# Kernel optimization log

Measured on AMD Instinct MI355X. Metric: run time of the kernel, lower is better.

The kernel has to match this reference:

```python
import jax, jax.numpy as jnp
import numpy as np
from jax import lax

NUM_HEADS = 3
HEAD_CH = 64  # in_ch // num_heads = 192 // 3
EPS = 1e-5   # haiku BatchNorm default eps


def _conv_proj(x, dw, scale, offset, pw, stride):
    # DepthwiseConv2D (SAME, no bias) -> BatchNorm (training: batch stats) -> 1x1 Conv (no bias)
    C = x.shape[-1]
    x = lax.conv_general_dilated(
        x, dw, (stride, stride), 'SAME',
        dimension_numbers=('NHWC', 'HWIO', 'NHWC'),
        feature_group_count=C)
    mean = x.mean(axis=(0, 1, 2))
    var = x.var(axis=(0, 1, 2))
    x = (x - mean) * lax.rsqrt(var + EPS) * scale + offset
    return jnp.einsum('bhwc,cd->bhwd', x, pw)  # pointwise 1x1 conv


def _split_heads(x):
    # b H W (h d) -> b h (H W) d
    b, hh, ww, c = x.shape
    return x.reshape(b, hh * ww, NUM_HEADS, HEAD_CH).transpose(0, 2, 1, 3)


def setup_inputs() -> dict:
    key = jax.random.key(0)
    ks = jax.random.split(key, 18)
    B, H, W, C = 16, 56, 56, 192
    Cout = NUM_HEADS * HEAD_CH  # 192
    g = lambda k, shape, s=0.02: jax.random.normal(k, shape, jnp.float32) * s
    return {
        'inputs_q':  jax.random.normal(ks[0], (B, H, W, C), jnp.float32),
        'inputs_kv': jax.random.normal(ks[1], (B, H, W, C), jnp.float32),
        # depthwise kernels (k, k, 1, C)
        'dw_q': g(ks[2], (3, 3, 1, C)), 'dw_k': g(ks[3], (3, 3, 1, C)), 'dw_v': g(ks[4], (3, 3, 1, C)),
        # BN scale/offset per projection
        'scale_q': jnp.ones((C,), jnp.float32), 'offset_q': jnp.zeros((C,), jnp.float32),
        'scale_k': jnp.ones((C,), jnp.float32), 'offset_k': jnp.zeros((C,), jnp.float32),
        'scale_v': jnp.ones((C,), jnp.float32), 'offset_v': jnp.zeros((C,), jnp.float32),
        # pointwise 1x1 conv kernels (C, Cout)
        'pw_q': g(ks[5], (C, Cout)), 'pw_k': g(ks[6], (C, Cout)), 'pw_v': g(ks[7], (C, Cout)),
        # talking-heads mixing matrices (h, h), near-identity init
        'pre_sm':  jnp.eye(NUM_HEADS, dtype=jnp.float32) + g(ks[8], (NUM_HEADS, NUM_HEADS), 0.1),
        'post_sm': jnp.eye(NUM_HEADS, dtype=jnp.float32) + g(ks[9], (NUM_HEADS, NUM_HEADS), 0.1),
        # output linear (no bias)
        'w_out': g(ks[10], (Cout, C)),
    }


def reference(inputs_q, inputs_kv, dw_q, dw_k, dw_v,
              scale_q, offset_q, scale_k, offset_k, scale_v, offset_v,
              pw_q, pw_k, pw_v, pre_sm, post_sm, w_out):
    q = _conv_proj(inputs_q,  dw_q, scale_q, offset_q, pw_q, 1)  # [B,56,56,192]
    k = _conv_proj(inputs_kv, dw_k, scale_k, offset_k, pw_k, 2)  # [B,28,28,192]
    v = _conv_proj(inputs_kv, dw_v, scale_v, offset_v, pw_v, 2)
    B = q.shape[0]
    q = _split_heads(q) / jnp.sqrt(jnp.float32(HEAD_CH))  # [B,h,Lq,d]
    k = _split_heads(k)                                   # [B,h,Lk,d]
    v = _split_heads(v)
    w = jnp.einsum('bhld,bhkd->bhlk', q, k)               # [B,h,Lq,Lk]
    w = jnp.einsum('bhlk,hg->bglk', w, pre_sm)            # pre-softmax talking heads
    w = jax.nn.softmax(w, axis=-1)
    w = jnp.einsum('bhlk,hg->bglk', w, post_sm)           # post-softmax talking heads
    s = jnp.einsum('bhlk,bhkd->bhld', w, v)               # [B,h,Lq,d]
    s = s.transpose(0, 2, 1, 3).reshape(B, -1, NUM_HEADS * HEAD_CH)  # b l (h d)
    return s @ w_out                                      # [B,Lq,192]
```

## Files before the change

### kernel.cpp

```cpp
#include <hip/hip_runtime.h>

using short8 = __attribute__((ext_vector_type(8))) short;
using f32x4  = __attribute__((ext_vector_type(4))) float;

__device__ __forceinline__ short f2bf(float f){
  unsigned u = __float_as_uint(f);
  unsigned r = (u + 0x7FFFu + ((u >> 16) & 1u)) >> 16;
  return (short)r;
}
__device__ __forceinline__ float sget(float x){
  return __uint_as_float(__builtin_amdgcn_readfirstlane(__float_as_uint(x)));
}
__device__ __forceinline__ unsigned cvtpk_bf16(float lo, float hi){
  unsigned d;
  asm("v_cvt_pk_bf16_f32 %0, %1, %2" : "=v"(d) : "v"(lo), "v"(hi));
  return d;
}
__device__ __forceinline__ void async_cp16(short* lds, const short* g){
  __builtin_amdgcn_global_load_lds((const __attribute__((address_space(1))) unsigned int*)g,
                                   (__attribute__((address_space(3))) unsigned int*)lds,
                                   16, 0, 0);
}

__global__ __launch_bounds__(384) void k_dw(const float* __restrict__ inq, const float* __restrict__ inkv,
                                            const float* __restrict__ wq, const float* __restrict__ wk,
                                            const float* __restrict__ wv,
                                            short* __restrict__ dqb, short* __restrict__ dkb,
                                            short* __restrict__ dvb, float2* __restrict__ partq,
                                            float2* __restrict__ partk, float2* __restrict__ partv){
  __shared__ float red[4][384];
  int t = threadIdx.x;
  int c = t % 192, strip = t / 192;
  if(blockIdx.x < 896){
    int bid = blockIdx.x; int b = bid / 56, oh = bid % 56;
    float w[9];
#pragma unroll
    for(int i=0;i<9;i++) w[i] = wq[i*192 + c];
    const float* inb = inq + (size_t)b*56*56*192;
    const float* rp[3]; bool rv[3];
#pragma unroll
    for(int kh=0;kh<3;kh++){
      int ih = oh + kh - 1;
      rv[kh] = (ih >= 0 && ih < 56);
      rp[kh] = inb + (size_t)(rv[kh] ? ih : 0)*56*192 + c;
    }
    auto ldc = [&](int kh, int iw)->float{
      return (rv[kh] && iw >= 0 && iw < 56) ? rp[kh][iw*192] : 0.f;
    };
    int ow0 = strip*28;
    float x0[3], x1[3];
#pragma unroll
    for(int kh=0;kh<3;kh++){ x0[kh] = ldc(kh, ow0-1); x1[kh] = ldc(kh, ow0); }
    float lsum = 0.f, lsq = 0.f;
    size_t orow = ((size_t)b*3136 + (size_t)oh*56)*192;
#pragma unroll 1
    for(int j=0;j<28;j++){
      int ow = ow0 + j;
      float x2[3];
#pragma unroll
      for(int kh=0;kh<3;kh++) x2[kh] = ldc(kh, ow+1);
      float acc = 0.f;
#pragma unroll
      for(int kh=0;kh<3;kh++){
        acc = fmaf(x0[kh], w[kh*3+0], acc);
        acc = fmaf(x1[kh], w[kh*3+1], acc);
        acc = fmaf(x2[kh], w[kh*3+2], acc);
      }
      dqb[orow + (size_t)ow*192 + c] = f2bf(acc);
      lsum += acc; lsq = fmaf(acc, acc, lsq);
#pragma unroll
      for(int kh=0;kh<3;kh++){ x0[kh] = x1[kh]; x1[kh] = x2[kh]; }
    }
    red[0][t] = lsum; red[1][t] = lsq;
    __syncthreads();
    if(t < 192){
      float2 o; o.x = lsum + red[0][t+192]; o.y = lsq + red[1][t+192];
      partq[(size_t)bid*192 + t] = o;
    }
  } else {
    int bid = blockIdx.x - 896; int b = bid / 28, oh = bid % 28;
    float wkr[9], wvr[9];
#pragma unroll
    for(int i=0;i<9;i++){ wkr[i] = wk[i*192 + c]; wvr[i] = wv[i*192 + c]; }
    const float* inb = inkv + (size_t)b*56*56*192;
    const float* rp[3]; bool rv[3];
#pragma unroll
    for(int kh=0;kh<3;kh++){
      int ih = 2*oh + kh;
      rv[kh] = (ih < 56);
      rp[kh] = inb + (size_t)(rv[kh] ? ih : 0)*56*192 + c;
    }
    auto ldc = [&](int kh, int iw)->float{
      return (rv[kh] && iw < 56) ? rp[kh][iw*192] : 0.f;
    };
    int ow0 = strip*14;
    float xp[3];
#pragma unroll
    for(int kh=0;kh<3;kh++) xp[kh] = ldc(kh, 2*ow0);
    float ksum=0.f, ksq=0.f, vsum=0.f, vsq=0.f;
    size_t orow = ((size_t)b*784 + (size_t)oh*28)*192;
#pragma unroll 1
    for(int j=0;j<14;j++){
      int ow = ow0 + j;
      float xm[3], xn[3];
#pragma unroll
      for(int kh=0;kh<3;kh++){ xm[kh] = ldc(kh, 2*ow+1); xn[kh] = ldc(kh, 2*ow+2); }
      float ak = 0.f, av = 0.f;
#pragma unroll
      for(int kh=0;kh<3;kh++){
        ak = fmaf(xp[kh], wkr[kh*3+0], ak); ak = fmaf(xm[kh], wkr[kh*3+1], ak); ak = fmaf(xn[kh], wkr[kh*3+2], ak);
        av = fmaf(xp[kh], wvr[kh*3+0], av); av = fmaf(xm[kh], wvr[kh*3+1], av); av = fmaf(xn[kh], wvr[kh*3+2], av);
      }
      dkb[orow + (size_t)ow*192 + c] = f2bf(ak);
      dvb[orow + (size_t)ow*192 + c] = f2bf(av);
      ksum += ak; ksq = fmaf(ak, ak, ksq);
      vsum += av; vsq = fmaf(av, av, vsq);
#pragma unroll
      for(int kh=0;kh<3;kh++) xp[kh] = xn[kh];
    }
    red[0][t]=ksum; red[1][t]=ksq; red[2][t]=vsum; red[3][t]=vsq;
    __syncthreads();
    if(t < 192){
      float2 a; a.x = ksum + red[0][t+192]; a.y = ksq + red[1][t+192];
      partk[(size_t)bid*192 + t] = a;
      float2 o; o.x = vsum + red[2][t+192]; o.y = vsq + red[3][t+192];
      partv[(size_t)bid*192 + t] = o;
    }
  }
}

__global__ __launch_bounds__(192) void k_red(const float2* __restrict__ pq, const float2* __restrict__ pk,
                                             const float2* __restrict__ pv, float2* __restrict__ oq,
                                             float2* __restrict__ ok2, float2* __restrict__ ov2){
  int blk = blockIdx.x, t = threadIdx.x;
  const float2* src; float2* dst;
  if(blk < 8){ src = pq + (size_t)blk*112*192;      dst = oq  + (size_t)blk*192; }
  else if(blk < 12){ src = pk + (size_t)(blk-8)*112*192;  dst = ok2 + (size_t)(blk-8)*192; }
  else { src = pv + (size_t)(blk-12)*112*192; dst = ov2 + (size_t)(blk-12)*192; }
  float s=0.f, q=0.f;
#pragma unroll 8
  for(int i=0;i<112;i++){ float2 v = src[(size_t)i*192 + t]; s += v.x; q += v.y; }
  float2 o; o.x=s; o.y=q; dst[t] = o;
}

__global__ __launch_bounds__(192) void k_fin(const float2* __restrict__ pq, const float2* __restrict__ pk,
                                             const float2* __restrict__ pv,
                                             const float* __restrict__ sq, const float* __restrict__ oq,
                                             const float* __restrict__ sk, const float* __restrict__ ok,
                                             const float* __restrict__ sv, const float* __restrict__ ov,
                                             const float* __restrict__ pwq, const float* __restrict__ pwk,
                                             const float* __restrict__ pwv, const float* __restrict__ wout,
                                             short* __restrict__ Wt, float* __restrict__ bias){
  int p = blockIdx.x, t = threadIdx.x;
  __shared__ float aS[192], bS[192];
  if(p < 3){
    const float2* part = (p==0)?pq:((p==1)?pk:pv);
    int nb = (p==0)?8:4;
    float N = (p==0)?50176.f:12544.f;
    const float* sc = (p==0)?sq:((p==1)?sk:sv);
    const float* of = (p==0)?oq:((p==1)?ok:ov);
    float s=0.f, q2=0.f;
#pragma unroll
    for(int i=0;i<8;i++){ if(i<nb){ float2 v = part[(size_t)i*192 + t]; s += v.x; q2 += v.y; } }
    float mean = s / N;
    float var  = q2 / N - mean*mean;
    float a  = rsqrtf(var + 1e-5f) * sc[t];
    float bv = of[t] - mean*a;
    aS[t] = a; bS[t] = bv;
    __syncthreads();
    const float* pw = (p==0)?pwq:((p==1)?pwk:pwv);
    float qs = (p==0) ? 0.125f : 1.0f;
    float bacc = 0.f;
    for(int cc=0; cc<192; cc++){
      float wv_ = pw[cc*192 + t];
      bacc = fmaf(bS[cc], wv_, bacc);
      Wt[((size_t)p*192 + t)*192 + cc] = f2bf(aS[cc]*wv_*qs);
    }
    bias[p*192 + t] = bacc * qs;
  } else {
    for(int cc=0; cc<192; cc++) Wt[((size_t)3*192 + t)*192 + cc] = f2bf(wout[cc*192 + t]);
    bias[3*192 + t] = 0.f;
  }
}

__global__ __launch_bounds__(256) void k_kv(const short* __restrict__ dkb, const short* __restrict__ dvb,
                                            const short* __restrict__ Wt, const float* __restrict__ bias,
                                            short* __restrict__ kbuf, short* __restrict__ vtb){
  int blk = blockIdx.x;
  bool isV = blk >= 208;
  int pb = isV ? blk - 208 : blk;
  int w = threadIdx.x >> 6, L = threadIdx.x & 63, l16 = L & 15, h4 = L >> 4;
  int row0 = pb*64 + w*16;
  int b = row0 / 832, kk0 = row0 - b*832;
  const short* A = isV ? dvb : dkb;
  const short* Wp = Wt + (isV ? 2 : 1)*36864;
  const float* bp = bias + (isV ? 2 : 1)*192;
  int kkA = kk0 + l16; if(kkA > 783) kkA = 783;
  short8 af[6];
  const short8* arow = (const short8*)(A + (size_t)(b*784 + kkA)*192);
#pragma unroll
  for(int kf=0;kf<6;kf++) af[kf] = arow[kf*4 + h4];
  short* obase = (isV ? vtb : kbuf) + (size_t)b*26*6144;
#pragma unroll
  for(int nt=0;nt<12;nt++){
    f32x4 acc = f32x4{0.f,0.f,0.f,0.f};
    const short8* wrow = (const short8*)(Wp + (size_t)(nt*16 + l16)*192);
#pragma unroll
    for(int kf=0;kf<6;kf++)
      acc = __builtin_amdgcn_mfma_f32_16x16x32_bf16(af[kf], wrow[kf*4 + h4], acc, 0,0,0);
    int col = nt*16 + l16;
    float bv = bp[col];
#pragma unroll
    for(int r=0;r<4;r++){
      int kk = kk0 + h4*4 + r;
      float v = (kk < 784) ? (acc[r] + bv) : 0.f;
      int t = kk >> 5, rr = kk & 31;
      if(!isV) obase[(size_t)t*6144 + (col>>3)*256 + rr*8 + (col&7)] = f2bf(v);
      else     obase[(size_t)t*6144 + (rr>>3)*1536 + col*8 + (rr&7)] = f2bf(v);
    }
  }
}

__global__ __launch_bounds__(256, 2) void k_attn(const short* __restrict__ dq, const short* __restrict__ Wt,
                                                 const float* __restrict__ bias,
                                                 const short* __restrict__ kb, const short* __restrict__ vt,
                                                 const float* __restrict__ pre, const float* __restrict__ post,
                                                 float* __restrict__ outp){
  __shared__ __align__(16) short sS[32256];
  short* sKb = sS;
  short* sVb = sS + 12288;
  short* sP  = sS + 24576;
  int bid = blockIdx.x;
  int b  = ((bid & 7) << 1) | ((bid >> 3) & 1);
  int lt = bid >> 4;
  int tid = threadIdx.x; int w = tid >> 6, lane = tid & 63, l16 = lane & 15, h4 = lane >> 4;
  int lw = lt*64 + w*16;
  short* sScr = sS + w*3200;

  {
    short8 af[6];
    const short8* arow = (const short8*)(dq + ((size_t)b*3136 + lw + l16)*192);
#pragma unroll
    for(int kf=0;kf<6;kf++) af[kf] = arow[kf*4 + h4];
#pragma unroll 1
    for(int nt=0;nt<12;nt++){
      f32x4 acc = f32x4{0.f,0.f,0.f,0.f};
      const short8* wrow = (const short8*)(Wt + (size_t)(nt*16 + l16)*192);
#pragma unroll
      for(int kf=0;kf<6;kf++)
        acc = __builtin_amdgcn_mfma_f32_16x16x32_bf16(af[kf], wrow[kf*4 + h4], acc, 0,0,0);
      float bv = bias[nt*16 + l16];
#pragma unroll
      for(int r=0;r<4;r++) sScr[(h4*4+r)*200 + nt*16 + l16] = f2bf(acc[r] + bv);
    }
  }
  short8 qf[3][2];
#pragma unroll
  for(int h=0;h<3;h++)
#pragma unroll
    for(int kf=0;kf<2;kf++) qf[h][kf] = *(const short8*)&sScr[l16*200 + h*64 + kf*32 + h4*8];

  float pm[3][3];
#pragma unroll
  for(int h=0;h<3;h++)
#pragma unroll
    for(int g=0;g<3;g++) pm[h][g] = sget(pre[h*3+g]) * 1.44269504f;

  f32x4 T[3][3][4];
#pragma unroll
  for(int g=0;g<3;g++)
#pragma unroll
    for(int gp=0;gp<3;gp++)
#pragma unroll
      for(int nt=0;nt<4;nt++) T[g][gp][nt] = f32x4{0.f,0.f,0.f,0.f};
  float Zp[3] = {0.f, 0.f, 0.f};

  const short* kgb = kb + (size_t)b*26*6144;
  const short* vgb = vt + (size_t)b*26*6144;
  int soff = w*1536;

  auto stage = [&](int t){
    short* kl = sKb + (t&1)*6144 + soff;
    short* vl = sVb + (t&1)*6144 + soff;
    const short* kg = kgb + (size_t)t*6144 + soff + lane*8;
    const short* vg = vgb + (size_t)t*6144 + soff + lane*8;
#pragma unroll
    for(int j=0;j<3;j++){
      async_cp16(kl + j*512, kg + j*512);
      async_cp16(vl + j*512, vg + j*512);
    }
  };

  __syncthreads();
  stage(0);
  __syncthreads();

  int sPw = w*1920;
#pragma unroll 1
  for(int ks=0; ks<25; ks++){
    if(ks < 24) stage(ks+1);
    const short* sKc = sKb + (ks&1)*6144;
    const short* sVc = sVb + (ks&1)*6144;
#pragma unroll
    for(int nt=0;nt<2;nt++){
      f32x4 a3[3];
#pragma unroll
      for(int h=0;h<3;h++) a3[h] = f32x4{0.f,0.f,0.f,0.f};
      __builtin_amdgcn_s_setprio(1);
#pragma unroll
      for(int h=0;h<3;h++)
#pragma unroll
        for(int kf=0;kf<2;kf++){
          short8 bk = *(const short8*)&sKc[(h*8 + kf*4 + h4)*256 + (nt*16 + l16)*8];
          a3[h] = __builtin_amdgcn_mfma_f32_16x16x32_bf16(bk, qf[h][kf], a3[h], 0,0,0);
        }
      __builtin_amdgcn_s_setprio(0);
      bool zok = (ks < 24) || (nt == 0);
#pragma unroll
      for(int g=0;g<3;g++){
        float e[4];
#pragma unroll
        for(int r=0;r<4;r++){
          float sm = fmaf(pm[0][g], a3[0][r], fmaf(pm[1][g], a3[1][r], pm[2][g]*a3[2][r]));
          e[r] = exp2f(sm);
        }
        if(zok) Zp[g] += (e[0] + e[1]) + (e[2] + e[3]);
        uint2 dw; dw.x = cvtpk_bf16(e[0], e[1]); dw.y = cvtpk_bf16(e[2], e[3]);
        *(uint2*)&sP[sPw + g*640 + l16*40 + nt*16 + h4*4] = dw;
      }
    }
    short8 pa[3];
#pragma unroll
    for(int g=0;g<3;g++) pa[g] = *(const short8*)&sP[sPw + g*640 + l16*40 + h4*8];
    __builtin_amdgcn_s_setprio(1);
#pragma unroll
    for(int gp=0;gp<3;gp++)
#pragma unroll
      for(int nt=0;nt<4;nt++){
        short8 vb = *(const short8*)&sVc[h4*1536 + (gp*64 + nt*16 + l16)*8];
#pragma unroll
        for(int g=0;g<3;g++)
          T[g][gp][nt] = __builtin_amdgcn_mfma_f32_16x16x32_bf16(pa[g], vb, T[g][gp][nt], 0,0,0);
      }
    __builtin_amdgcn_s_setprio(0);
    __syncthreads();
  }

  float izq[3][4];
#pragma unroll
  for(int g=0;g<3;g++){
    float z = Zp[g];
    z += __shfl_xor(z, 16); z += __shfl_xor(z, 32);
    float iz = 1.f / z;
#pragma unroll
    for(int r=0;r<4;r++) izq[g][r] = __shfl(iz, h4*4 + r);
  }
  float po[3][3];
#pragma unroll
  for(int g=0;g<3;g++)
#pragma unroll
    for(int gp=0;gp<3;gp++) po[g][gp] = sget(post[g*3+gp]);

#pragma unroll
  for(int gp=0;gp<3;gp++){
    float cg[3][4];
#pragma unroll
    for(int g=0;g<3;g++)
#pragma unroll
      for(int r=0;r<4;r++) cg[g][r] = po[g][gp] * izq[g][r];
#pragma unroll
    for(int nt=0;nt<4;nt++){
#pragma unroll
      for(int r=0;r<4;r++){
        float u = fmaf(cg[0][r], T[0][gp][nt][r], fmaf(cg[1][r], T[1][gp][nt][r], cg[2][r]*T[2][gp][nt][r]));
        sScr[(h4*4+r)*200 + gp*64 + nt*16 + l16] = f2bf(u);
      }
    }
  }
  short8 uf[6];
#pragma unroll
  for(int kf=0;kf<6;kf++) uf[kf] = *(const short8*)&sScr[l16*200 + kf*32 + h4*8];
  const short* W3 = Wt + 3*36864;
#pragma unroll 1
  for(int nt=0;nt<12;nt++){
    f32x4 acc = f32x4{0.f,0.f,0.f,0.f};
    const short8* wrow = (const short8*)(W3 + (size_t)(nt*16 + l16)*192);
#pragma unroll
    for(int kf=0;kf<6;kf++)
      acc = __builtin_amdgcn_mfma_f32_16x16x32_bf16(uf[kf], wrow[kf*4 + h4], acc, 0,0,0);
#pragma unroll
    for(int r=0;r<4;r++)
      outp[((size_t)b*3136 + lw + h4*4 + r)*192 + nt*16 + l16] = acc[r];
  }
}

extern "C" void kernel_launch(void* const* d_in, const int* in_sizes, int n_in,
                              void* d_out, int out_size, void* d_ws, size_t ws_size,
                              hipStream_t stream){
  (void)in_sizes; (void)n_in; (void)out_size; (void)ws_size;
  const float* inq  = (const float*)d_in[0];
  const float* inkv = (const float*)d_in[1];
  const float* dwq  = (const float*)d_in[2];
  const float* dwk  = (const float*)d_in[3];
  const float* dwv  = (const float*)d_in[4];
  const float* scq  = (const float*)d_in[5];  const float* ofq = (const float*)d_in[6];
  const float* sck  = (const float*)d_in[7];  const float* ofk = (const float*)d_in[8];
  const float* scv  = (const float*)d_in[9];  const float* ofv = (const float*)d_in[10];
  const float* pwq  = (const float*)d_in[11];
  const float* pwk  = (const float*)d_in[12];
  const float* pwv  = (const float*)d_in[13];
  const float* pre  = (const float*)d_in[14];
  const float* post = (const float*)d_in[15];
  const float* wout = (const float*)d_in[16];

  char* ws = (char*)d_ws;
  size_t off = 0;
  auto alloc = [&](size_t bytes)->void*{ void* p = ws + off; off += (bytes + 255) & ~(size_t)255; return p; };
  short*  dqb  = (short*) alloc(50176ull*192*2);
  short*  dkb  = (short*) alloc(12544ull*192*2);
  short*  dvb  = (short*) alloc(12544ull*192*2);
  short*  kbuf = (short*) alloc(16ull*26*6144*2);
  short*  vtb  = (short*) alloc(16ull*26*6144*2);
  float2* pq   = (float2*)alloc(896ull*192*sizeof(float2));
  float2* pk   = (float2*)alloc(448ull*192*sizeof(float2));
  float2* pv   = (float2*)alloc(448ull*192*sizeof(float2));
  float2* pq2  = (float2*)alloc(8ull*192*sizeof(float2));
  float2* pk2  = (float2*)alloc(4ull*192*sizeof(float2));
  float2* pv2  = (float2*)alloc(4ull*192*sizeof(float2));
  short*  Wt   = (short*) alloc(4ull*192*192*2);
  float*  bias = (float*) alloc(4ull*192*4);

  k_dw<<<1344, 384, 0, stream>>>(inq, inkv, dwq, dwk, dwv, dqb, dkb, dvb, pq, pk, pv);
  k_red<<<16, 192, 0, stream>>>(pq, pk, pv, pq2, pk2, pv2);
  k_fin<<<4, 192, 0, stream>>>(pq2, pk2, pv2, scq, ofq, sck, ofk, scv, ofv, pwq, pwk, pwv, wout, Wt, bias);
  k_kv<<<416, 256, 0, stream>>>(dkb, dvb, Wt, bias, kbuf, vtb);
  k_attn<<<784, 256, 0, stream>>>(dqb, Wt, bias, kbuf, vtb, pre, post, (float*)d_out);
}
```

Baseline: 237.7 us.

## Split attention into two passes to apply post-softmax mixing before PV

The single pass that accumulated nine un-normalized PV accumulators (one per pre/post head pair) becomes two passes. The first pass computes QK and the softmax denominators only. The second recomputes QK, normalizes, mixes the heads with the post-softmax matrix, and runs PV with just three accumulators. This cuts PV MFMAs by a factor of three and lowers accumulator register pressure, but doubles the QK MFMAs and exp work and reads K twice.

```diff
diff --git a/kernel.cpp b/kernel.cpp
--- a/kernel.cpp
+++ b/kernel.cpp
@@ -266,20 +266,17 @@
 #pragma unroll
     for(int g=0;g<3;g++) pm[h][g] = sget(pre[h*3+g]) * 1.44269504f;
 
-  f32x4 T[3][3][4];
-#pragma unroll
-  for(int g=0;g<3;g++)
-#pragma unroll
-    for(int gp=0;gp<3;gp++)
-#pragma unroll
-      for(int nt=0;nt<4;nt++) T[g][gp][nt] = f32x4{0.f,0.f,0.f,0.f};
-  float Zp[3] = {0.f, 0.f, 0.f};
-
   const short* kgb = kb + (size_t)b*26*6144;
   const short* vgb = vt + (size_t)b*26*6144;
   int soff = w*1536;
 
-  auto stage = [&](int t){
+  auto stageK = [&](int t){
+    short* kl = sKb + (t&1)*6144 + soff;
+    const short* kg = kgb + (size_t)t*6144 + soff + lane*8;
+#pragma unroll
+    for(int j=0;j<3;j++) async_cp16(kl + j*512, kg + j*512);
+  };
+  auto stageKV = [&](int t){
     short* kl = sKb + (t&1)*6144 + soff;
     short* vl = sVb + (t&1)*6144 + soff;
     const short* kg = kgb + (size_t)t*6144 + soff + lane*8;
@@ -291,16 +288,15 @@
     }
   };
 
+  float Zp[3] = {0.f, 0.f, 0.f};
   __syncthreads();
-  stage(0);
+  stageK(0);
   __syncthreads();
 
-  int sPw = w*1920;
 #pragma unroll 1
   for(int ks=0; ks<25; ks++){
-    if(ks < 24) stage(ks+1);
+    if(ks < 24) stageK(ks+1);
     const short* sKc = sKb + (ks&1)*6144;
-    const short* sVc = sVb + (ks&1)*6144;
 #pragma unroll
     for(int nt=0;nt<2;nt++){
       f32x4 a3[3];
@@ -318,65 +314,98 @@
       bool zok = (ks < 24) || (nt == 0);
 #pragma unroll
       for(int g=0;g<3;g++){
-        float e[4];
+        float e0 = exp2f(fmaf(pm[0][g], a3[0][0], fmaf(pm[1][g], a3[1][0], pm[2][g]*a3[2][0])));
+        float e1 = exp2f(fmaf(pm[0][g], a3[0][1], fmaf(pm[1][g], a3[1][1], pm[2][g]*a3[2][1])));
+        float e2 = exp2f(fmaf(pm[0][g], a3[0][2], fmaf(pm[1][g], a3[1][2], pm[2][g]*a3[2][2])));
+        float e3 = exp2f(fmaf(pm[0][g], a3[0][3], fmaf(pm[1][g], a3[1][3], pm[2][g]*a3[2][3])));
+        if(zok) Zp[g] += (e0 + e1) + (e2 + e3);
+      }
+    }
+    __syncthreads();
+  }
+
+  float izq[3];
+#pragma unroll
+  for(int g=0;g<3;g++){
+    float z = Zp[g];
+    z += __shfl_xor(z, 16); z += __shfl_xor(z, 32);
+    izq[g] = 1.f / z;
+  }
+  float po[3][3];
+#pragma unroll
+  for(int g=0;g<3;g++)
+#pragma unroll
+    for(int gp=0;gp<3;gp++) po[g][gp] = sget(post[g*3+gp]);
+
+  f32x4 U[3][4];
+#pragma unroll
+  for(int gp=0;gp<3;gp++)
+#pragma unroll
+    for(int nt=0;nt<4;nt++) U[gp][nt] = f32x4{0.f,0.f,0.f,0.f};
+
+  stageKV(0);
+  __syncthreads();
+
+  int sPw = w*1920;
+#pragma unroll 1
+  for(int ks=0; ks<25; ks++){
+    if(ks < 24) stageKV(ks+1);
+    const short* sKc = sKb + (ks&1)*6144;
+    const short* sVc = sVb + (ks&1)*6144;
+#pragma unroll
+    for(int nt=0;nt<2;nt++){
+      f32x4 a3[3];
+#pragma unroll
+      for(int h=0;h<3;h++) a3[h] = f32x4{0.f,0.f,0.f,0.f};
+      __builtin_amdgcn_s_setprio(1);
+#pragma unroll
+      for(int h=0;h<3;h++)
+#pragma unroll
+        for(int kf=0;kf<2;kf++){
+          short8 bk = *(const short8*)&sKc[(h*8 + kf*4 + h4)*256 + (nt*16 + l16)*8];
+          a3[h] = __builtin_amdgcn_mfma_f32_16x16x32_bf16(bk, qf[h][kf], a3[h], 0,0,0);
+        }
+      __builtin_amdgcn_s_setprio(0);
+      float pn[3][4];
+#pragma unroll
+      for(int g=0;g<3;g++)
 #pragma unroll
         for(int r=0;r<4;r++){
           float sm = fmaf(pm[0][g], a3[0][r], fmaf(pm[1][g], a3[1][r], pm[2][g]*a3[2][r]));
-          e[r] = exp2f(sm);
+          pn[g][r] = exp2f(sm) * izq[g];
         }
-        if(zok) Zp[g] += (e[0] + e[1]) + (e[2] + e[3]);
-        uint2 dw; dw.x = cvtpk_bf16(e[0], e[1]); dw.y = cvtpk_bf16(e[2], e[3]);
-        *(uint2*)&sP[sPw + g*640 + l16*40 + nt*16 + h4*4] = dw;
+#pragma unroll
+      for(int gp=0;gp<3;gp++){
+        float w0 = fmaf(po[0][gp], pn[0][0], fmaf(po[1][gp], pn[1][0], po[2][gp]*pn[2][0]));
+        float w1 = fmaf(po[0][gp], pn[0][1], fmaf(po[1][gp], pn[1][1], po[2][gp]*pn[2][1]));
+        float w2 = fmaf(po[0][gp], pn[0][2], fmaf(po[1][gp], pn[1][2], po[2][gp]*pn[2][2]));
+        float w3 = fmaf(po[0][gp], pn[0][3], fmaf(po[1][gp], pn[1][3], po[2][gp]*pn[2][3]));
+        uint2 dw; dw.x = cvtpk_bf16(w0, w1); dw.y = cvtpk_bf16(w2, w3);
+        *(uint2*)&sP[sPw + gp*640 + l16*40 + nt*16 + h4*4] = dw;
       }
     }
     short8 pa[3];
 #pragma unroll
-    for(int g=0;g<3;g++) pa[g] = *(const short8*)&sP[sPw + g*640 + l16*40 + h4*8];
+    for(int gp=0;gp<3;gp++) pa[gp] = *(const short8*)&sP[sPw + gp*640 + l16*40 + h4*8];
     __builtin_amdgcn_s_setprio(1);
 #pragma unroll
     for(int gp=0;gp<3;gp++)
 #pragma unroll
       for(int nt=0;nt<4;nt++){
         short8 vb = *(const short8*)&sVc[h4*1536 + (gp*64 + nt*16 + l16)*8];
-#pragma unroll
-        for(int g=0;g<3;g++)
-          T[g][gp][nt] = __builtin_amdgcn_mfma_f32_16x16x32_bf16(pa[g], vb, T[g][gp][nt], 0,0,0);
+        U[gp][nt] = __builtin_amdgcn_mfma_f32_16x16x32_bf16(pa[gp], vb, U[gp][nt], 0,0,0);
       }
     __builtin_amdgcn_s_setprio(0);
     __syncthreads();
   }
 
-  float izq[3][4];
-#pragma unroll
-  for(int g=0;g<3;g++){
-    float z = Zp[g];
-    z += __shfl_xor(z, 16); z += __shfl_xor(z, 32);
-    float iz = 1.f / z;
-#pragma unroll
-    for(int r=0;r<4;r++) izq[g][r] = __shfl(iz, h4*4 + r);
-  }
-  float po[3][3];
-#pragma unroll
-  for(int g=0;g<3;g++)
-#pragma unroll
-    for(int gp=0;gp<3;gp++) po[g][gp] = sget(post[g*3+gp]);
-
-#pragma unroll
-  for(int gp=0;gp<3;gp++){
-    float cg[3][4];
-#pragma unroll
-    for(int g=0;g<3;g++)
-#pragma unroll
-      for(int r=0;r<4;r++) cg[g][r] = po[g][gp] * izq[g][r];
-#pragma unroll
-    for(int nt=0;nt<4;nt++){
-#pragma unroll
-      for(int r=0;r<4;r++){
-        float u = fmaf(cg[0][r], T[0][gp][nt][r], fmaf(cg[1][r], T[1][gp][nt][r], cg[2][r]*T[2][gp][nt][r]));
-        sScr[(h4*4+r)*200 + gp*64 + nt*16 + l16] = f2bf(u);
-      }
-    }
-  }
+#pragma unroll
+  for(int gp=0;gp<3;gp++)
+#pragma unroll
+    for(int nt=0;nt<4;nt++)
+#pragma unroll
+      for(int r=0;r<4;r++)
+        sScr[(h4*4+r)*200 + gp*64 + nt*16 + l16] = f2bf(U[gp][nt][r]);
   short8 uf[6];
 #pragma unroll
   for(int kf=0;kf<6;kf++) uf[kf] = *(const short8*)&sScr[l16*200 + kf*32 + h4*8];
```

New measurement: 283.3 us. +19.2%, slower.
